# Kernel tuning notes

Measured on AMD Instinct MI355X. Metric: run time of the kernel, lower is better.

Reference implementation:

```python
import jax, jax.numpy as jnp
import numpy as np

B, T, C = 4, 2048, 1024
H = 16
HS = C // H  # 64
FF = 4 * C
EPS = 1e-5


def setup_inputs() -> dict:
    key = jax.random.key(0)
    ks = jax.random.split(key, 12)
    s = lambda k, shape, fan: jax.random.normal(k, shape, jnp.float32) * (fan ** -0.5)
    return {
        "x": jax.random.normal(ks[0], (B, T, C), jnp.float32),
        "Wq": s(ks[1], (H, C, HS), C),
        "Wk": s(ks[2], (H, C, HS), C),
        "Wv": s(ks[3], (H, C, HS), C),
        "Wproj": s(ks[4], (C, C), C),
        "bproj": jnp.zeros((C,), jnp.float32),
        "W1": s(ks[5], (C, FF), C),
        "b1": jnp.zeros((FF,), jnp.float32),
        "W2": s(ks[6], (FF, C), FF),
        "b2": jnp.zeros((C,), jnp.float32),
        "g1": jnp.ones((C,), jnp.float32),
        "be1": jnp.zeros((C,), jnp.float32),
        "g2": jnp.ones((C,), jnp.float32),
        "be2": jnp.zeros((C,), jnp.float32),
    }


def _layernorm(x, g, b):
    mu = jnp.mean(x, axis=-1, keepdims=True)
    var = jnp.mean(jnp.square(x - mu), axis=-1, keepdims=True)
    return (x - mu) * jax.lax.rsqrt(var + EPS) * g + b


def reference(x, Wq, Wk, Wv, Wproj, bproj, W1, b1, W2, b2, g1, be1, g2, be2):
    # --- multi-head causal self-attention on ln1(x) ---
    h = _layernorm(x, g1, be1)                      # [B,T,C]
    q = jnp.einsum("btc,hcd->bhtd", h, Wq)
    k = jnp.einsum("btc,hcd->bhtd", h, Wk)
    v = jnp.einsum("btc,hcd->bhtd", h, Wv)
    scores = jnp.einsum("bhtd,bhsd->bhts", q, k) * (HS ** -0.5)  # [B,H,T,T]
    causal = jnp.tril(jnp.ones((T, T), bool))
    scores = jnp.where(causal, scores, -jnp.inf)
    wei = jax.nn.softmax(scores, axis=-1)
    attn = jnp.einsum("bhts,bhsd->bhtd", wei, v)    # [B,H,T,HS]
    attn = attn.transpose(0, 2, 1, 3).reshape(B, T, C)  # concat heads
    x = x + attn @ Wproj + bproj
    # --- feed-forward on ln2(x) ---
    h2 = _layernorm(x, g2, be2)
    x = x + jax.nn.relu(h2 @ W1 + b1) @ W2 + b2
    return x
```

## Files before the change

### kernel.cpp

```cpp
#include <hip/hip_runtime.h>
#include <hip/hip_bf16.h>
#include <stdint.h>


typedef unsigned short u16;
typedef __bf16 bf16x8 __attribute__((ext_vector_type(8)));
typedef float f32x4 __attribute__((ext_vector_type(4)));
typedef float f32x16 __attribute__((ext_vector_type(16)));

#define MFMA16(a, b, c) __builtin_amdgcn_mfma_f32_16x16x32_bf16((a), (b), (c), 0, 0, 0)
#define MFMA32(a, b, c) __builtin_amdgcn_mfma_f32_32x32x16_bf16((a), (b), (c), 0, 0, 0)

__device__ __forceinline__ u16 f2bf(float f) {
  __hip_bfloat16 h = __float2bfloat16(f);
  return __builtin_bit_cast(u16, h);
}

__device__ __forceinline__ float bf2f(u16 u) {
  uint32_t t = (uint32_t)u << 16;
  return __builtin_bit_cast(float, t);
}

__device__ __forceinline__ uint32_t cvtpk(float lo, float hi_) {
  uint32_t r;
  asm("v_cvt_pk_bf16_f32 %0, %1, %2" : "=v"(r) : "v"(lo), "v"(hi_));
  return r;
}

__device__ __forceinline__ void pl32swap(uint32_t& a, uint32_t& b) {
  asm("v_permlane32_swap_b32 %0, %1" : "+v"(a), "+v"(b));
}

__device__ __forceinline__ void gload16(const void* g, void* l) {
  __builtin_amdgcn_global_load_lds(
      (__attribute__((address_space(1))) void*)g,
      (__attribute__((address_space(3))) void*)l, 16, 0, 0);
}

__global__ __launch_bounds__(256) void ln_kernel(
    const float* __restrict__ x, const float* __restrict__ g,
    const float* __restrict__ be, u16* __restrict__ out) {
  const int row = blockIdx.x;
  const int tid = threadIdx.x;
  const float4 v = reinterpret_cast<const float4*>(x + (size_t)row * 1024)[tid];
  float s = v.x + v.y + v.z + v.w;
  float s2 = v.x * v.x + v.y * v.y + v.z * v.z + v.w * v.w;
#pragma unroll
  for (int off = 1; off < 64; off <<= 1) {
    s += __shfl_xor(s, off);
    s2 += __shfl_xor(s2, off);
  }
  __shared__ float red[8];
  const int wid = tid >> 6;
  if ((tid & 63) == 0) { red[wid] = s; red[4 + wid] = s2; }
  __syncthreads();
  s = red[0] + red[1] + red[2] + red[3];
  s2 = red[4] + red[5] + red[6] + red[7];
  const float mu = s * (1.0f / 1024.0f);
  const float rstd = rsqrtf(s2 * (1.0f / 1024.0f) - mu * mu + 1e-5f);
  const float4 gv = reinterpret_cast<const float4*>(g)[tid];
  const float4 bv = reinterpret_cast<const float4*>(be)[tid];
  ushort4 o;
  o.x = f2bf((v.x - mu) * rstd * gv.x + bv.x);
  o.y = f2bf((v.y - mu) * rstd * gv.y + bv.y);
  o.z = f2bf((v.z - mu) * rstd * gv.z + bv.z);
  o.w = f2bf((v.w - mu) * rstd * gv.w + bv.w);
  *reinterpret_cast<ushort4*>(out + (size_t)row * 1024 + tid * 4) = o;
}

__global__ __launch_bounds__(256) void tcvt(
    const float* __restrict__ src, u16* __restrict__ dst,
    int R, int C, size_t sstride, size_t dstride) {
  src += (size_t)blockIdx.z * sstride;
  dst += (size_t)blockIdx.z * dstride;
  __shared__ float t[64][65];
  const int r0 = blockIdx.x * 64, c0 = blockIdx.y * 64;
  const int tid = threadIdx.x;
  const int cc = tid & 63, rr = tid >> 6;
#pragma unroll
  for (int p = 0; p < 16; ++p) {
    const int r = rr + p * 4;
    t[r][cc] = src[(size_t)(r0 + r) * C + c0 + cc];
  }
  __syncthreads();
#pragma unroll
  for (int p = 0; p < 16; ++p) {
    const int c = rr + p * 4;
    dst[(size_t)(c0 + c) * R + r0 + cc] = f2bf(t[cc][c]);
  }
}

__global__ __launch_bounds__(256) void ff2_combine(
    const u16* __restrict__ p0, const u16* __restrict__ p1,
    const float* __restrict__ b2, float* __restrict__ out) {
  const size_t base = ((size_t)blockIdx.x * 256 + threadIdx.x) * 8;
  const uint4 a0 = *reinterpret_cast<const uint4*>(p0 + base);
  const uint4 a1 = *reinterpret_cast<const uint4*>(p1 + base);
  const u16* e0 = reinterpret_cast<const u16*>(&a0);
  const u16* e1 = reinterpret_cast<const u16*>(&a1);
  const int c = (int)(base & 1023);
  const float4 bv0 = *reinterpret_cast<const float4*>(b2 + c);
  const float4 bv1 = *reinterpret_cast<const float4*>(b2 + c + 4);
  float4 o0 = *reinterpret_cast<const float4*>(out + base);
  float4 o1 = *reinterpret_cast<const float4*>(out + base + 4);
  o0.x += bf2f(e0[0]) + bf2f(e1[0]) + bv0.x;
  o0.y += bf2f(e0[1]) + bf2f(e1[1]) + bv0.y;
  o0.z += bf2f(e0[2]) + bf2f(e1[2]) + bv0.z;
  o0.w += bf2f(e0[3]) + bf2f(e1[3]) + bv0.w;
  o1.x += bf2f(e0[4]) + bf2f(e1[4]) + bv1.x;
  o1.y += bf2f(e0[5]) + bf2f(e1[5]) + bv1.y;
  o1.z += bf2f(e0[6]) + bf2f(e1[6]) + bv1.z;
  o1.w += bf2f(e0[7]) + bf2f(e1[7]) + bv1.w;
  *reinterpret_cast<float4*>(out + base) = o0;
  *reinterpret_cast<float4*>(out + base + 4) = o1;
}

constexpr int EPI_QKV = 0;
constexpr int EPI_RES = 1;
constexpr int EPI_RELU = 2;
constexpr int EPI_PART = 3;

template <int EPI>
__global__ __launch_bounds__(512) void gemm256(
    const u16* __restrict__ A, const u16* __restrict__ Bt,
    int M, int N, int Kloop, int Kstride, int NBN, int SPLIT,
    u16* outB, u16* outB2, float* outF, const float* bias) {
  __shared__ u16 sA[2][256 * 64] __attribute__((aligned(16)));
  __shared__ u16 sB[2][256 * 64] __attribute__((aligned(16)));
  const int tid = threadIdx.x;
  const int lane = tid & 63, wid = tid >> 6;
  const int wr = wid >> 2, wc = wid & 3;
  const int l16 = lane & 15, lg = lane >> 4;
  const int nwg = gridDim.x;
  const int wgid = (blockIdx.x & 7) * (nwg >> 3) + (blockIdx.x >> 3);
  int wg = wgid, ks = 0;
  if (SPLIT) { ks = wg & 1; wg >>= 1; }
  const int bm = wg / NBN, bn = wg % NBN;
  const u16* Ap = A + (size_t)ks * Kloop;
  const u16* Btp = Bt + (size_t)ks * Kloop;
  u16* outp = (SPLIT && ks) ? outB2 : outB;
  const size_t rowA = (size_t)bm * 256;
  const size_t rowB = (size_t)bn * 256;
  const int nkt = Kloop >> 6;

  f32x4 acc[8][4];
#pragma unroll
  for (int m = 0; m < 8; ++m)
#pragma unroll
    for (int n = 0; n < 4; ++n) {
      acc[m][n][0] = 0.f; acc[m][n][1] = 0.f; acc[m][n][2] = 0.f; acc[m][n][3] = 0.f;
    }

  auto stageA = [&](int kt, int h) {
    if (kt >= nkt) return;
    const int k0 = kt << 6;
    char* base = (char*)&sA[kt & 1][h * 8192];
#pragma unroll
    for (int it = 0; it < 2; ++it) {
      const int f = tid + it * 512;
      const int r = f >> 3, c = f & 7;
      gload16(Ap + (rowA + h * 128 + r) * Kstride + k0 + ((c ^ (r & 7)) << 3), base + f * 16);
    }
  };
  auto stageB = [&](int kt, int h) {
    if (kt >= nkt) return;
    const int k0 = kt << 6;
    char* base = (char*)&sB[kt & 1][h * 8192];
#pragma unroll
    for (int it = 0; it < 2; ++it) {
      const int f = tid + it * 512;
      const int r = f >> 3, c = f & 7;
      gload16(Btp + (rowB + h * 128 + r) * Kstride + k0 + ((c ^ (r & 7)) << 3), base + f * 16);
    }
  };

  stageA(0, 0); stageB(0, 0); stageA(0, 1); stageB(0, 1);
  stageB(1, 0); stageA(1, 0);
  asm volatile("s_waitcnt vmcnt(4)" ::: "memory");
  __builtin_amdgcn_s_barrier();
  asm volatile("" ::: "memory");

  bf16x8 a[4][2], b[4][2];
  for (int kt = 0; kt < nkt; ++kt) {
    const u16* bufA = &sA[kt & 1][0];
    const u16* bufB = &sB[kt & 1][0];
#pragma unroll
    for (int m = 0; m < 4; ++m)
#pragma unroll
      for (int kk = 0; kk < 2; ++kk) {
        const int r = wr * 128 + m * 16 + l16;
        a[m][kk] = *reinterpret_cast<const bf16x8*>(bufA + r * 64 + (((kk * 4 + lg) ^ (r & 7)) << 3));
      }
#pragma unroll
    for (int n = 0; n < 2; ++n)
#pragma unroll
      for (int kk = 0; kk < 2; ++kk) {
        const int r = wc * 64 + n * 16 + l16;
        b[n][kk] = *reinterpret_cast<const bf16x8*>(bufB + r * 64 + (((kk * 4 + lg) ^ (r & 7)) << 3));
      }
    stageB(kt + 1, 1);
    __builtin_amdgcn_s_barrier();
    asm volatile("s_waitcnt lgkmcnt(0)" ::: "memory");
    __builtin_amdgcn_s_setprio(1);
#pragma unroll
    for (int kk = 0; kk < 2; ++kk)
#pragma unroll
      for (int m = 0; m < 4; ++m)
#pragma unroll
        for (int n = 0; n < 2; ++n)
          acc[m][n] = MFMA16(a[m][kk], b[n][kk], acc[m][n]);
    __builtin_amdgcn_s_setprio(0);
    __builtin_amdgcn_s_barrier();
    asm volatile("" ::: "memory");
#pragma unroll
    for (int n = 2; n < 4; ++n)
#pragma unroll
      for (int kk = 0; kk < 2; ++kk) {
        const int r = wc * 64 + n * 16 + l16;
        b[n][kk] = *reinterpret_cast<const bf16x8*>(bufB + r * 64 + (((kk * 4 + lg) ^ (r & 7)) << 3));
      }
    stageA(kt + 1, 1);
    __builtin_amdgcn_s_barrier();
    asm volatile("s_waitcnt lgkmcnt(0)" ::: "memory");
    __builtin_amdgcn_s_setprio(1);
#pragma unroll
    for (int kk = 0; kk < 2; ++kk)
#pragma unroll
      for (int m = 0; m < 4; ++m)
#pragma unroll
        for (int n = 2; n < 4; ++n)
          acc[m][n] = MFMA16(a[m][kk], b[n][kk], acc[m][n]);
    __builtin_amdgcn_s_setprio(0);
    __builtin_amdgcn_s_barrier();
    asm volatile("" ::: "memory");
#pragma unroll
    for (int m = 0; m < 4; ++m)
#pragma unroll
      for (int kk = 0; kk < 2; ++kk) {
        const int r = wr * 128 + 64 + m * 16 + l16;
        a[m][kk] = *reinterpret_cast<const bf16x8*>(bufA + r * 64 + (((kk * 4 + lg) ^ (r & 7)) << 3));
      }
    stageB(kt + 2, 0);
    __builtin_amdgcn_s_barrier();
    asm volatile("s_waitcnt lgkmcnt(0)" ::: "memory");
    __builtin_amdgcn_s_setprio(1);
#pragma unroll
    for (int kk = 0; kk < 2; ++kk)
#pragma unroll
      for (int m = 0; m < 4; ++m)
#pragma unroll
        for (int n = 2; n < 4; ++n)
          acc[4 + m][n] = MFMA16(a[m][kk], b[n][kk], acc[4 + m][n]);
    __builtin_amdgcn_s_setprio(0);
    __builtin_amdgcn_s_barrier();
    asm volatile("" ::: "memory");
    stageA(kt + 2, 0);
    __builtin_amdgcn_s_setprio(1);
#pragma unroll
    for (int kk = 0; kk < 2; ++kk)
#pragma unroll
      for (int m = 0; m < 4; ++m)
#pragma unroll
        for (int n = 0; n < 2; ++n)
          acc[4 + m][n] = MFMA16(a[m][kk], b[n][kk], acc[4 + m][n]);
    __builtin_amdgcn_s_setprio(0);
    if (kt + 2 < nkt) {
      asm volatile("s_waitcnt vmcnt(4)" ::: "memory");
    } else {
      asm volatile("s_waitcnt vmcnt(0)" ::: "memory");
    }
    __builtin_amdgcn_s_barrier();
    asm volatile("" ::: "memory");
  }

#pragma unroll
  for (int m = 0; m < 8; ++m)
#pragma unroll
    for (int n = 0; n < 4; ++n)
#pragma unroll
      for (int ii = 0; ii < 4; ++ii) {
        const int gi = bm * 256 + wr * 128 + m * 16 + lg * 4 + ii;
        const int gj = bn * 256 + wc * 64 + n * 16 + l16;
        const float val = acc[m][n][ii];
        if constexpr (EPI == EPI_QKV) {
          const int sel = gj >> 10;
          const int hh = (gj >> 6) & 15;
          const int dd = gj & 63;
          const int bb = gi >> 11, tt = gi & 2047;
          const float sv = (sel == 0) ? val * 0.1803368801f : val;
          outB[(size_t)sel * 8388608 + ((size_t)(bb * 16 + hh) * 2048 + tt) * 64 + dd] = f2bf(sv);
        } else if constexpr (EPI == EPI_RELU) {
          const float bv = val + bias[gj];
          outB[(size_t)gi * N + gj] = f2bf(bv > 0.f ? bv : 0.f);
        } else if constexpr (EPI == EPI_PART) {
          outp[(size_t)gi * N + gj] = f2bf(val);
        }
      }
}

template <int EPI>
__global__ __launch_bounds__(512) void gemm128(
    const u16* __restrict__ A, const u16* __restrict__ Bt,
    int M, int N, int K, int NBN,
    u16* outB, float* outF, const float* bias, const float* res) {
  __shared__ u16 sA[2][128 * 64] __attribute__((aligned(16)));
  __shared__ u16 sB[2][256 * 64] __attribute__((aligned(16)));
  const int tid = threadIdx.x;
  const int lane = tid & 63, wid = tid >> 6;
  const int wr = wid >> 2, wc = wid & 3;
  const int l16 = lane & 15, lg = lane >> 4;
  const int nwg = gridDim.x;
  const int wgid = (blockIdx.x & 7) * (nwg >> 3) + (blockIdx.x >> 3);
  const int bm = wgid / NBN, bn = wgid % NBN;
  const size_t rowA = (size_t)bm * 128;
  const size_t rowB = (size_t)bn * 256;
  const int nkt = K >> 6;

  f32x4 acc[4][4];
#pragma unroll
  for (int m = 0; m < 4; ++m)
#pragma unroll
    for (int n = 0; n < 4; ++n) {
      acc[m][n][0] = 0.f; acc[m][n][1] = 0.f; acc[m][n][2] = 0.f; acc[m][n][3] = 0.f;
    }

  auto stageA = [&](int kt, int h) {
    if (kt >= nkt) return;
    const int k0 = kt << 6;
    char* base = (char*)&sA[kt & 1][h * 4096];
    const int r = tid >> 3, c = tid & 7;
    gload16(A + (rowA + h * 64 + r) * K + k0 + ((c ^ (r & 7)) << 3), base + tid * 16);
  };
  auto stageB = [&](int kt, int h) {
    if (kt >= nkt) return;
    const int k0 = kt << 6;
    char* base = (char*)&sB[kt & 1][h * 8192];
#pragma unroll
    for (int it = 0; it < 2; ++it) {
      const int f = tid + it * 512;
      const int r = f >> 3, c = f & 7;
      gload16(Bt + (rowB + h * 128 + r) * K + k0 + ((c ^ (r & 7)) << 3), base + f * 16);
    }
  };

  stageA(0, 0); stageB(0, 0); stageA(0, 1); stageB(0, 1);
  stageB(1, 0); stageA(1, 0);
  asm volatile("s_waitcnt vmcnt(3)" ::: "memory");
  __builtin_amdgcn_s_barrier();
  asm volatile("" ::: "memory");

  bf16x8 a[2][2], b[4][2];
  for (int kt = 0; kt < nkt; ++kt) {
    const u16* bufA = &sA[kt & 1][0];
    const u16* bufB = &sB[kt & 1][0];
#pragma unroll
    for (int m = 0; m < 2; ++m)
#pragma unroll
      for (int kk = 0; kk < 2; ++kk) {
        const int r = wr * 64 + m * 16 + l16;
        a[m][kk] = *reinterpret_cast<const bf16x8*>(bufA + r * 64 + (((kk * 4 + lg) ^ (r & 7)) << 3));
      }
#pragma unroll
    for (int n = 0; n < 2; ++n)
#pragma unroll
      for (int kk = 0; kk < 2; ++kk) {
        const int r = wc * 64 + n * 16 + l16;
        b[n][kk] = *reinterpret_cast<const bf16x8*>(bufB + r * 64 + (((kk * 4 + lg) ^ (r & 7)) << 3));
      }
    stageB(kt + 1, 1);
    __builtin_amdgcn_s_barrier();
    asm volatile("s_waitcnt lgkmcnt(0)" ::: "memory");
    __builtin_amdgcn_s_setprio(1);
#pragma unroll
    for (int kk = 0; kk < 2; ++kk)
#pragma unroll
      for (int m = 0; m < 2; ++m)
#pragma unroll
        for (int n = 0; n < 2; ++n)
          acc[m][n] = MFMA16(a[m][kk], b[n][kk], acc[m][n]);
    __builtin_amdgcn_s_setprio(0);
    __builtin_amdgcn_s_barrier();
    asm volatile("" ::: "memory");
#pragma unroll
    for (int n = 2; n < 4; ++n)
#pragma unroll
      for (int kk = 0; kk < 2; ++kk) {
        const int r = wc * 64 + n * 16 + l16;
        b[n][kk] = *reinterpret_cast<const bf16x8*>(bufB + r * 64 + (((kk * 4 + lg) ^ (r & 7)) << 3));
      }
    stageA(kt + 1, 1);
    __builtin_amdgcn_s_barrier();
    asm volatile("s_waitcnt lgkmcnt(0)" ::: "memory");
    __builtin_amdgcn_s_setprio(1);
#pragma unroll
    for (int kk = 0; kk < 2; ++kk)
#pragma unroll
      for (int m = 0; m < 2; ++m)
#pragma unroll
        for (int n = 2; n < 4; ++n)
          acc[m][n] = MFMA16(a[m][kk], b[n][kk], acc[m][n]);
    __builtin_amdgcn_s_setprio(0);
    __builtin_amdgcn_s_barrier();
    asm volatile("" ::: "memory");
#pragma unroll
    for (int m = 0; m < 2; ++m)
#pragma unroll
      for (int kk = 0; kk < 2; ++kk) {
        const int r = wr * 64 + (m + 2) * 16 + l16;
        a[m][kk] = *reinterpret_cast<const bf16x8*>(bufA + r * 64 + (((kk * 4 + lg) ^ (r & 7)) << 3));
      }
    stageB(kt + 2, 0);
    __builtin_amdgcn_s_barrier();
    asm volatile("s_waitcnt lgkmcnt(0)" ::: "memory");
    __builtin_amdgcn_s_setprio(1);
#pragma unroll
    for (int kk = 0; kk < 2; ++kk)
#pragma unroll
      for (int m = 0; m < 2; ++m)
#pragma unroll
        for (int n = 2; n < 4; ++n)
          acc[2 + m][n] = MFMA16(a[m][kk], b[n][kk], acc[2 + m][n]);
    __builtin_amdgcn_s_setprio(0);
    __builtin_amdgcn_s_barrier();
    asm volatile("" ::: "memory");
    stageA(kt + 2, 0);
    __builtin_amdgcn_s_setprio(1);
#pragma unroll
    for (int kk = 0; kk < 2; ++kk)
#pragma unroll
      for (int m = 0; m < 2; ++m)
#pragma unroll
        for (int n = 0; n < 2; ++n)
          acc[2 + m][n] = MFMA16(a[m][kk], b[n][kk], acc[2 + m][n]);
    __builtin_amdgcn_s_setprio(0);
    if (kt + 2 < nkt) {
      asm volatile("s_waitcnt vmcnt(3)" ::: "memory");
    } else {
      asm volatile("s_waitcnt vmcnt(0)" ::: "memory");
    }
    __builtin_amdgcn_s_barrier();
    asm volatile("" ::: "memory");
  }

#pragma unroll
  for (int m = 0; m < 4; ++m)
#pragma unroll
    for (int n = 0; n < 4; ++n)
#pragma unroll
      for (int ii = 0; ii < 4; ++ii) {
        const int gi = bm * 128 + wr * 64 + m * 16 + lg * 4 + ii;
        const int gj = bn * 256 + wc * 64 + n * 16 + l16;
        const float val = acc[m][n][ii];
        if constexpr (EPI == EPI_RES) {
          const size_t idx = (size_t)gi * N + gj;
          outF[idx] = val + bias[gj] + res[idx];
        }
      }
}

__global__ __launch_bounds__(256, 3) void attn_kernel(
    const u16* __restrict__ q, const u16* __restrict__ k,
    const u16* __restrict__ v, u16* __restrict__ o) {
  const int bid = blockIdx.x;
  const int bh = (bid & 7) * 8 + ((bid >> 3) & 7);
  const int qt = 15 - (bid >> 6);
  const int tid = threadIdx.x;
  const int lane = tid & 63, wid = tid >> 6;
  const int l32 = lane & 31, hi = lane >> 5;
  const u16* qb = q + (size_t)bh * (2048 * 64);
  const u16* kb = k + (size_t)bh * (2048 * 64);
  const u16* vb = v + (size_t)bh * (2048 * 64);
  const int q0 = qt * 128;
  const int qrow = q0 + wid * 32 + l32;

  __shared__ u16 sK[2][64 * 64] __attribute__((aligned(16)));
  __shared__ u16 sVt[2][64 * 72] __attribute__((aligned(16)));

  bf16x8 bq[4];
#pragma unroll
  for (int s = 0; s < 4; ++s)
    bq[s] = *reinterpret_cast<const bf16x8*>(qb + (size_t)qrow * 64 + s * 16 + hi * 8);

  f32x16 oacc[2];
#pragma unroll
  for (int r = 0; r < 16; ++r) { oacc[0][r] = 0.f; oacc[1][r] = 0.f; }
  float mi = -1e30f, li = 0.f;

  uint4 vr0, vr1;

  auto stageK = [&](int s0, int buf) {
#pragma unroll
    for (int it = 0; it < 2; ++it) {
      const int f = tid + it * 256;
      const int r = f >> 3, c = f & 7;
      gload16(kb + (size_t)(s0 + r) * 64 + (size_t)((c ^ (r & 7)) * 8),
              (char*)&sK[buf][0] + it * 4096 + wid * 1024);
    }
  };
  auto loadV = [&](int s0) {
    const int kvp = tid & 31;
    const int c8 = tid >> 5;
    vr0 = *reinterpret_cast<const uint4*>(vb + (size_t)(s0 + 2 * kvp) * 64 + c8 * 8);
    vr1 = *reinterpret_cast<const uint4*>(vb + (size_t)(s0 + 2 * kvp + 1) * 64 + c8 * 8);
  };
  auto writeV = [&](int buf) {
    const int kvp = tid & 31;
    const int c8 = tid >> 5;
    const u16* e0 = reinterpret_cast<const u16*>(&vr0);
    const u16* e1 = reinterpret_cast<const u16*>(&vr1);
    u16* base = &sVt[buf][0];
#pragma unroll
    for (int j = 0; j < 8; ++j) {
      const int d = c8 * 8 + j;
      *reinterpret_cast<uint32_t*>(base + d * 72 + 2 * kvp) =
          (uint32_t)e0[j] | ((uint32_t)e1[j] << 16);
    }
  };

  const int nst = 2 * qt + 2;
  stageK(0, 0);
  loadV(0);
  asm volatile("s_waitcnt vmcnt(0)" ::: "memory");
  writeV(0);
  __syncthreads();

  int cur = 0;
  for (int ks = 0; ks < nst; ++ks) {
    const int s0 = ks * 64;
    const int nxt = cur ^ 1;
    if (ks + 1 < nst) { stageK(s0 + 64, nxt); loadV(s0 + 64); }

    f32x16 st[2];
#pragma unroll
    for (int r = 0; r < 16; ++r) { st[0][r] = 0.f; st[1][r] = 0.f; }
#pragma unroll
    for (int t = 0; t < 2; ++t) {
      const int row = t * 32 + l32;
      const int rx = row & 7;
#pragma unroll
      for (int s = 0; s < 4; ++s) {
        bf16x8 ak = *reinterpret_cast<const bf16x8*>(
            &sK[cur][0] + row * 64 + (((s * 2 + hi) ^ rx) << 3));
        st[t] = MFMA32(ak, bq[s], st[t]);
      }
    }

    if (ks >= 2 * qt) {
#pragma unroll
      for (int t = 0; t < 2; ++t)
#pragma unroll
        for (int a = 0; a < 4; ++a)
#pragma unroll
          for (int c2 = 0; c2 < 4; ++c2) {
            const int kvg = s0 + t * 32 + a * 8 + hi * 4 + c2;
            if (kvg > qrow) st[t][a * 4 + c2] = -1e30f;
          }
    }

    float pm = -3e38f;
#pragma unroll
    for (int t = 0; t < 2; ++t)
#pragma unroll
      for (int r = 0; r < 16; ++r) pm = fmaxf(pm, st[t][r]);
    pm = fmaxf(pm, __shfl_xor(pm, 32));
    if (__any(pm > mi)) {
      const float mn = fmaxf(mi, pm);
      const float al = exp2f(mi - mn);
      mi = mn;
      li *= al;
#pragma unroll
      for (int dt = 0; dt < 2; ++dt)
#pragma unroll
        for (int r = 0; r < 16; ++r) oacc[dt][r] *= al;
    }
    float rs = 0.f;
#pragma unroll
    for (int t = 0; t < 2; ++t)
#pragma unroll
      for (int r = 0; r < 16; ++r) {
        const float p = exp2f(st[t][r] - mi);
        st[t][r] = p;
        rs += p;
      }
    rs += __shfl_xor(rs, 32);
    li += rs;

    uint32_t W[2][4][2];
#pragma unroll
    for (int t = 0; t < 2; ++t)
#pragma unroll
      for (int a = 0; a < 4; ++a) {
        W[t][a][0] = cvtpk(st[t][a * 4 + 0], st[t][a * 4 + 1]);
        W[t][a][1] = cvtpk(st[t][a * 4 + 2], st[t][a * 4 + 3]);
      }
#pragma unroll
    for (int ks2 = 0; ks2 < 4; ++ks2) {
      const int t = ks2 >> 1;
      uint32_t A0 = W[t][(2 * ks2) & 3][0], B0 = W[t][(2 * ks2 + 1) & 3][0];
      uint32_t A1 = W[t][(2 * ks2) & 3][1], B1 = W[t][(2 * ks2 + 1) & 3][1];
      pl32swap(A0, B0);
      pl32swap(A1, B1);
      union { uint32_t w[4]; bf16x8 v; } bp;
      bp.w[0] = A0; bp.w[1] = A1; bp.w[2] = B0; bp.w[3] = B1;
#pragma unroll
      for (int dt = 0; dt < 2; ++dt) {
        bf16x8 av = *reinterpret_cast<const bf16x8*>(
            &sVt[cur][0] + (dt * 32 + l32) * 72 + ks2 * 16 + hi * 8);
        oacc[dt] = MFMA32(av, bp.v, oacc[dt]);
      }
    }

    if (ks + 1 < nst) {
      asm volatile("s_waitcnt vmcnt(0)" ::: "memory");
      writeV(nxt);
      __syncthreads();
    }
    cur = nxt;
  }

  const int bb = bh >> 4, hh = bh & 15;
  const float rli = 1.0f / li;
  const size_t rowo = (size_t)(bb * 2048 + qrow) * 1024;
#pragma unroll
  for (int dt = 0; dt < 2; ++dt)
#pragma unroll
    for (int a = 0; a < 4; ++a) {
      ushort4 pk;
      pk.x = f2bf(oacc[dt][a * 4 + 0] * rli);
      pk.y = f2bf(oacc[dt][a * 4 + 1] * rli);
      pk.z = f2bf(oacc[dt][a * 4 + 2] * rli);
      pk.w = f2bf(oacc[dt][a * 4 + 3] * rli);
      *reinterpret_cast<ushort4*>(o + rowo + hh * 64 + dt * 32 + a * 8 + hi * 4) = pk;
    }
}

extern "C" void kernel_launch(void* const* d_in, const int* in_sizes, int n_in,
                              void* d_out, int out_size, void* d_ws, size_t ws_size,
                              hipStream_t stream) {
  const float* x = (const float*)d_in[0];
  const float* Wq = (const float*)d_in[1];
  const float* Wk = (const float*)d_in[2];
  const float* Wv = (const float*)d_in[3];
  const float* Wproj = (const float*)d_in[4];
  const float* bproj = (const float*)d_in[5];
  const float* W1 = (const float*)d_in[6];
  const float* b1 = (const float*)d_in[7];
  const float* W2 = (const float*)d_in[8];
  const float* b2 = (const float*)d_in[9];
  const float* g1 = (const float*)d_in[10];
  const float* be1 = (const float*)d_in[11];
  const float* g2 = (const float*)d_in[12];
  const float* be2 = (const float*)d_in[13];
  float* out = (float*)d_out;

  char* ws = (char*)d_ws;
  const size_t MB16 = 16777216ull;
  u16* hb = (u16*)(ws);
  u16* qkv = (u16*)(ws + MB16);
  u16* qp = qkv;
  u16* kp = qkv + 8388608;
  u16* vp = qkv + 2 * 8388608;
  u16* ab = (u16*)(ws + 4 * MB16);
  u16* f1 = qkv;
  u16* wqkvt = (u16*)(ws + 5 * MB16);
  u16* wprojt = wqkvt + 3145728;
  u16* w1t = wprojt + 1048576;
  u16* w2t = w1t + 4194304;
  u16* p0 = hb;
  u16* p1 = wqkvt;

  dim3 blk(256);
  tcvt<<<dim3(16, 1, 16), blk, 0, stream>>>(Wq, wqkvt, 1024, 64, 65536, 65536);
  tcvt<<<dim3(16, 1, 16), blk, 0, stream>>>(Wk, wqkvt + 1048576, 1024, 64, 65536, 65536);
  tcvt<<<dim3(16, 1, 16), blk, 0, stream>>>(Wv, wqkvt + 2097152, 1024, 64, 65536, 65536);
  tcvt<<<dim3(16, 16, 1), blk, 0, stream>>>(Wproj, wprojt, 1024, 1024, 0, 0);
  tcvt<<<dim3(16, 64, 1), blk, 0, stream>>>(W1, w1t, 1024, 4096, 0, 0);
  tcvt<<<dim3(64, 16, 1), blk, 0, stream>>>(W2, w2t, 4096, 1024, 0, 0);

  ln_kernel<<<8192, blk, 0, stream>>>(x, g1, be1, hb);
  gemm256<EPI_QKV><<<384, 512, 0, stream>>>(hb, wqkvt, 8192, 3072, 1024, 1024, 12, 0,
                                            qkv, nullptr, nullptr, nullptr);
  attn_kernel<<<1024, blk, 0, stream>>>(qp, kp, vp, ab);
  gemm128<EPI_RES><<<256, 512, 0, stream>>>(ab, wprojt, 8192, 1024, 1024, 4,
                                            nullptr, out, bproj, x);
  ln_kernel<<<8192, blk, 0, stream>>>(out, g2, be2, hb);
  gemm256<EPI_RELU><<<512, 512, 0, stream>>>(hb, w1t, 8192, 4096, 1024, 1024, 16, 0,
                                             f1, nullptr, nullptr, b1);
  gemm256<EPI_PART><<<256, 512, 0, stream>>>(f1, w2t, 8192, 1024, 2048, 4096, 4, 1,
                                             p0, p1, nullptr, nullptr);
  ff2_combine<<<4096, blk, 0, stream>>>(p0, p1, b2, out);
}
```

Before: 373.8 us.

## Fuse weight conversion with LN1, rebalance attention tiles, compute row sums via MFMA

Merges the six weight transpose/convert launches and the first layernorm into a single prep kernel, so fewer launches and no gaps between small kernels. The attention kernel now takes its query tiles from a reordered table so heavy and light causal tiles are interleaved across waves. It also computes the softmax denominator with an extra MFMA against a ones vector instead of a VALU sum plus shuffle, and uses a tree reduction for the row max. The extra MFMA per step adds matrix work in exchange for less scalar reduction.

```diff
diff --git a/kernel.cpp b/kernel.cpp
--- a/kernel.cpp
+++ b/kernel.cpp
@@ -37,11 +37,9 @@
       (__attribute__((address_space(3))) void*)l, 16, 0, 0);
 }
 
-__global__ __launch_bounds__(256) void ln_kernel(
-    const float* __restrict__ x, const float* __restrict__ g,
-    const float* __restrict__ be, u16* __restrict__ out) {
-  const int row = blockIdx.x;
-  const int tid = threadIdx.x;
+__device__ __forceinline__ void ln_body(
+    int row, int tid, const float* __restrict__ x, const float* __restrict__ g,
+    const float* __restrict__ be, u16* __restrict__ out, float* red) {
   const float4 v = reinterpret_cast<const float4*>(x + (size_t)row * 1024)[tid];
   float s = v.x + v.y + v.z + v.w;
   float s2 = v.x * v.x + v.y * v.y + v.z * v.z + v.w * v.w;
@@ -50,7 +48,6 @@
     s += __shfl_xor(s, off);
     s2 += __shfl_xor(s2, off);
   }
-  __shared__ float red[8];
   const int wid = tid >> 6;
   if ((tid & 63) == 0) { red[wid] = s; red[4 + wid] = s2; }
   __syncthreads();
@@ -68,14 +65,49 @@
   *reinterpret_cast<ushort4*>(out + (size_t)row * 1024 + tid * 4) = o;
 }
 
-__global__ __launch_bounds__(256) void tcvt(
-    const float* __restrict__ src, u16* __restrict__ dst,
-    int R, int C, size_t sstride, size_t dstride) {
-  src += (size_t)blockIdx.z * sstride;
-  dst += (size_t)blockIdx.z * dstride;
+__global__ __launch_bounds__(256) void ln_kernel(
+    const float* __restrict__ x, const float* __restrict__ g,
+    const float* __restrict__ be, u16* __restrict__ out) {
+  __shared__ float red[8];
+  ln_body(blockIdx.x, threadIdx.x, x, g, be, out, red);
+}
+
+__global__ __launch_bounds__(256) void prep(
+    const float* __restrict__ x, const float* __restrict__ g1,
+    const float* __restrict__ be1, u16* __restrict__ hb,
+    const float* __restrict__ Wq, const float* __restrict__ Wk,
+    const float* __restrict__ Wv, const float* __restrict__ Wproj,
+    const float* __restrict__ W1, const float* __restrict__ W2,
+    u16* __restrict__ wqkvt, u16* __restrict__ wprojt,
+    u16* __restrict__ w1t, u16* __restrict__ w2t) {
   __shared__ float t[64][65];
-  const int r0 = blockIdx.x * 64, c0 = blockIdx.y * 64;
   const int tid = threadIdx.x;
+  int b = blockIdx.x;
+  if (b < 8192) {
+    ln_body(b, tid, x, g1, be1, hb, &t[0][0]);
+    return;
+  }
+  b -= 8192;
+  const float* src;
+  u16* dst;
+  int R, C, bx, by;
+  if (b < 768) {
+    const int w = b >> 8, r = b & 255;
+    const int z = r >> 4;
+    src = (w == 0 ? Wq : w == 1 ? Wk : Wv) + (size_t)z * 65536;
+    dst = wqkvt + w * 1048576 + (size_t)z * 65536;
+    R = 1024; C = 64; bx = r & 15; by = 0;
+  } else if (b < 1024) {
+    const int r = b - 768;
+    src = Wproj; dst = wprojt; R = 1024; C = 1024; bx = r & 15; by = r >> 4;
+  } else if (b < 2048) {
+    const int r = b - 1024;
+    src = W1; dst = w1t; R = 1024; C = 4096; bx = r & 15; by = r >> 4;
+  } else {
+    const int r = b - 2048;
+    src = W2; dst = w2t; R = 4096; C = 1024; bx = r & 63; by = r >> 6;
+  }
+  const int r0 = bx * 64, c0 = by * 64;
   const int cc = tid & 63, rr = tid >> 6;
 #pragma unroll
   for (int p = 0; p < 16; ++p) {
@@ -458,12 +490,15 @@
       }
 }
 
+__device__ __constant__ int QTAB[16] = {15, 14, 13, 12, 11, 10, 9, 8,
+                                        4, 5, 6, 7, 0, 1, 2, 3};
+
 __global__ __launch_bounds__(256, 3) void attn_kernel(
     const u16* __restrict__ q, const u16* __restrict__ k,
     const u16* __restrict__ v, u16* __restrict__ o) {
   const int bid = blockIdx.x;
   const int bh = (bid & 7) * 8 + ((bid >> 3) & 7);
-  const int qt = 15 - (bid >> 6);
+  const int qt = QTAB[bid >> 6];
   const int tid = threadIdx.x;
   const int lane = tid & 63, wid = tid >> 6;
   const int l32 = lane & 31, hi = lane >> 5;
@@ -481,10 +516,19 @@
   for (int s = 0; s < 4; ++s)
     bq[s] = *reinterpret_cast<const bf16x8*>(qb + (size_t)qrow * 64 + s * 16 + hi * 8);
 
-  f32x16 oacc[2];
-#pragma unroll
-  for (int r = 0; r < 16; ++r) { oacc[0][r] = 0.f; oacc[1][r] = 0.f; }
-  float mi = -1e30f, li = 0.f;
+  bf16x8 aone;
+  {
+    union { u16 u[8]; bf16x8 v; } onec;
+    const u16 ov = (l32 == 0) ? (u16)0x3F80 : (u16)0;
+#pragma unroll
+    for (int j = 0; j < 8; ++j) onec.u[j] = ov;
+    aone = onec.v;
+  }
+
+  f32x16 oacc[2], osum;
+#pragma unroll
+  for (int r = 0; r < 16; ++r) { oacc[0][r] = 0.f; oacc[1][r] = 0.f; osum[r] = 0.f; }
+  float mi = -1e30f;
 
   uint4 vr0, vr1;
 
@@ -557,33 +601,28 @@
           }
     }
 
-    float pm = -3e38f;
-#pragma unroll
-    for (int t = 0; t < 2; ++t)
-#pragma unroll
-      for (int r = 0; r < 16; ++r) pm = fmaxf(pm, st[t][r]);
-    pm = fmaxf(pm, __shfl_xor(pm, 32));
+    float tm[16];
+#pragma unroll
+    for (int r = 0; r < 16; ++r) tm[r] = fmaxf(st[0][r], st[1][r]);
+#pragma unroll
+    for (int s2 = 8; s2 >= 1; s2 >>= 1)
+#pragma unroll
+      for (int r = 0; r < s2; ++r) tm[r] = fmaxf(tm[r], tm[r + s2]);
+    const float pm = fmaxf(tm[0], __shfl_xor(tm[0], 32));
     if (__any(pm > mi)) {
       const float mn = fmaxf(mi, pm);
       const float al = exp2f(mi - mn);
       mi = mn;
-      li *= al;
+      osum[0] *= al;
 #pragma unroll
       for (int dt = 0; dt < 2; ++dt)
 #pragma unroll
         for (int r = 0; r < 16; ++r) oacc[dt][r] *= al;
     }
-    float rs = 0.f;
 #pragma unroll
     for (int t = 0; t < 2; ++t)
 #pragma unroll
-      for (int r = 0; r < 16; ++r) {
-        const float p = exp2f(st[t][r] - mi);
-        st[t][r] = p;
-        rs += p;
-      }
-    rs += __shfl_xor(rs, 32);
-    li += rs;
+      for (int r = 0; r < 16; ++r) st[t][r] = exp2f(st[t][r] - mi);
 
     uint32_t W[2][4][2];
 #pragma unroll
@@ -608,6 +647,7 @@
             &sVt[cur][0] + (dt * 32 + l32) * 72 + ks2 * 16 + hi * 8);
         oacc[dt] = MFMA32(av, bp.v, oacc[dt]);
       }
+      osum = MFMA32(aone, bp.v, osum);
     }
 
     if (ks + 1 < nst) {
@@ -618,6 +658,7 @@
     cur = nxt;
   }
 
+  const float li = __shfl(osum[0], l32);
   const int bb = bh >> 4, hh = bh & 15;
   const float rli = 1.0f / li;
   const size_t rowo = (size_t)(bb * 2048 + qrow) * 1024;
@@ -670,14 +711,8 @@
   u16* p1 = wqkvt;
 
   dim3 blk(256);
-  tcvt<<<dim3(16, 1, 16), blk, 0, stream>>>(Wq, wqkvt, 1024, 64, 65536, 65536);
-  tcvt<<<dim3(16, 1, 16), blk, 0, stream>>>(Wk, wqkvt + 1048576, 1024, 64, 65536, 65536);
-  tcvt<<<dim3(16, 1, 16), blk, 0, stream>>>(Wv, wqkvt + 2097152, 1024, 64, 65536, 65536);
-  tcvt<<<dim3(16, 16, 1), blk, 0, stream>>>(Wproj, wprojt, 1024, 1024, 0, 0);
-  tcvt<<<dim3(16, 64, 1), blk, 0, stream>>>(W1, w1t, 1024, 4096, 0, 0);
-  tcvt<<<dim3(64, 16, 1), blk, 0, stream>>>(W2, w2t, 4096, 1024, 0, 0);
-
-  ln_kernel<<<8192, blk, 0, stream>>>(x, g1, be1, hb);
+  prep<<<11264, blk, 0, stream>>>(x, g1, be1, hb, Wq, Wk, Wv, Wproj, W1, W2,
+                                  wqkvt, wprojt, w1t, w2t);
   gemm256<EPI_QKV><<<384, 512, 0, stream>>>(hb, wqkvt, 8192, 3072, 1024, 1024, 12, 0,
                                             qkv, nullptr, nullptr, nullptr);
   attn_kernel<<<1024, blk, 0, stream>>>(qp, kp, vp, ab);
```

New measurement: 364.4 us. 1.03x faster.
